# Performance work log

Hardware: AMD Instinct MI355X
Metric: run time of the kernel (lower is better)

Reference implementation:

```python
import jax, jax.numpy as jnp
import numpy as np

B, D_IN, D_OUT, M = 4096, 1024, 1024, 16
GAMMA = 2.0


def setup_inputs() -> dict:
    key = jax.random.key(0)
    ks = jax.random.split(key, 5)
    scale_in = 1.0 / np.sqrt(D_IN)
    return {
        "x": jax.random.normal(ks[0], (B, D_IN), dtype=jnp.float32),
        "W": jax.random.normal(ks[1], (M, D_IN, D_OUT), dtype=jnp.float32) * scale_in,
        "b": jax.random.normal(ks[2], (M, D_OUT), dtype=jnp.float32) * 0.01,
        "Wg": jax.random.normal(ks[3], (D_IN, M), dtype=jnp.float32) * scale_in,
        "bg": jax.random.normal(ks[4], (M,), dtype=jnp.float32) * 0.01,
    }


def reference(x, W, b, Wg, bg):
    # Gate: linear -> pow(gamma) -> normalize by row sum -> relu
    gu = x @ Wg + bg                                   # [B, M]
    gp = jnp.power(gu, GAMMA)                          # gamma = 2.0
    gates = jax.nn.relu(gp / jnp.sum(gp, axis=1, keepdims=True))  # [B, M]
    # M dense expert modules: relu(x @ W_m + b_m), gated and summed (AdditionSublayer)
    h = jax.nn.relu(jnp.einsum("bi,mio->bmo", x, W) + b)          # [B, M, D_OUT]
    return jnp.einsum("bm,bmo->bo", gates, h)                     # [B, D_OUT]
```

## Files before the change

### kernel.cpp

```cpp
#include <hip/hip_runtime.h>

typedef unsigned short u16;
typedef __attribute__((ext_vector_type(4))) float f32x4;
typedef __attribute__((ext_vector_type(8))) short bf16x8;
typedef __attribute__((ext_vector_type(4))) unsigned short u16x4;

#define NT2 256

__device__ __forceinline__ u16 f2bf(float f) {
  union { float f; unsigned u; } v; v.f = f;
  unsigned r = v.u + 0x7FFFu + ((v.u >> 16) & 1u);
  return (u16)(r >> 16);
}

__device__ __forceinline__ f32x4 zero4() {
  f32x4 z; z.x = 0.f; z.y = 0.f; z.z = 0.f; z.w = 0.f; return z;
}

__global__ __launch_bounds__(256) void k_cvt_x(const float* __restrict__ x, u16* __restrict__ xb) {
  int i = blockIdx.x * 256 + threadIdx.x;
  f32x4 v = ((const f32x4*)x)[i];
  u16x4 o;
  o.x = f2bf(v.x); o.y = f2bf(v.y); o.z = f2bf(v.z); o.w = f2bf(v.w);
  ((u16x4*)xb)[i] = o;
}

__global__ __launch_bounds__(256) void k_tw(const float* __restrict__ W, u16* __restrict__ wt) {
  __shared__ float t[64][65];
  int bid = blockIdx.x;
  int e = bid >> 8, rem = bid & 255, kt = rem >> 4, nt = rem & 15;
  int tid = threadIdx.x;
  int lr = tid >> 4, lc4 = (tid & 15) * 4;
  const float* src = W + (size_t)e * 1048576 + (size_t)(kt * 64) * 1024 + nt * 64;
  #pragma unroll
  for (int i = 0; i < 4; ++i) {
    int r = lr + i * 16;
    f32x4 v = *(const f32x4*)(src + (size_t)r * 1024 + lc4);
    t[r][lc4] = v.x; t[r][lc4 + 1] = v.y; t[r][lc4 + 2] = v.z; t[r][lc4 + 3] = v.w;
  }
  __syncthreads();
  int sr = tid >> 3, sc0 = (tid & 7) * 8;
  u16* dst = wt + (size_t)e * 1048576 + (size_t)(nt * 64) * 1024 + kt * 64;
  #pragma unroll
  for (int i = 0; i < 2; ++i) {
    int r2 = sr + i * 32;
    union { u16 u[8]; bf16x8 v; } o;
    #pragma unroll
    for (int j = 0; j < 8; ++j) o.u[j] = f2bf(t[sc0 + j][r2]);
    *(bf16x8*)(dst + (size_t)r2 * 1024 + sc0) = o.v;
  }
}

__global__ __launch_bounds__(256) void k_gates(const float* __restrict__ x, const float* __restrict__ Wg,
                                               const float* __restrict__ bg, float* __restrict__ gates) {
  int wid = threadIdx.x >> 6, lane = threadIdx.x & 63;
  int b = blockIdx.x * 4 + wid;
  const float* xr = x + (size_t)b * 1024;
  float acc[16];
  #pragma unroll
  for (int m = 0; m < 16; ++m) acc[m] = 0.f;
  for (int i0 = lane * 4; i0 < 1024; i0 += 256) {
    f32x4 xv = *(const f32x4*)(xr + i0);
    #pragma unroll
    for (int j = 0; j < 4; ++j) {
      float xs = xv[j];
      const f32x4* wg = (const f32x4*)(Wg + (size_t)(i0 + j) * 16);
      #pragma unroll
      for (int q = 0; q < 4; ++q) {
        f32x4 w = wg[q];
        acc[q*4+0] += xs * w.x; acc[q*4+1] += xs * w.y;
        acc[q*4+2] += xs * w.z; acc[q*4+3] += xs * w.w;
      }
    }
  }
  #pragma unroll
  for (int m = 0; m < 16; ++m) {
    #pragma unroll
    for (int off = 32; off > 0; off >>= 1)
      acc[m] += __shfl_xor(acc[m], off, 64);
  }
  float tot = 0.f, gp[16];
  #pragma unroll
  for (int m = 0; m < 16; ++m) { float gu = acc[m] + bg[m]; gp[m] = gu * gu; tot += gp[m]; }
  float inv = 1.f / tot;
  if (lane == 0) {
    #pragma unroll
    for (int m = 0; m < 16; ++m) gates[(size_t)b * 16 + m] = gp[m] * inv;
  }
}

#define GLL(srcaddr, ldsaddr) \
  __builtin_amdgcn_global_load_lds((const __attribute__((address_space(1))) void*)(srcaddr), \
                                   (__attribute__((address_space(3))) void*)(ldsaddr), 16, 0, 0)

__global__ __launch_bounds__(256, 2)
void k_moe(const u16* __restrict__ xb, const u16* __restrict__ wt,
           const float* __restrict__ gates, const float* __restrict__ bias,
           float* __restrict__ out0, float* __restrict__ p1out) {
  __shared__ __align__(16) u16 sA[3 * 4096];
  __shared__ __align__(16) u16 sB[3 * 4096];
  __shared__ float lgat[1024];
  __shared__ float lbias[1024];

  int tid = threadIdx.x;
  int bid = blockIdx.x;
  int swz = (bid & 7) * 64 + (bid >> 3);
  int btile = swz & 31;
  int pnl = swz >> 5;
  int ntile = pnl & 7;
  int grp = pnl >> 3;
  int brow0 = btile * 128;
  int ncol0 = ntile * 128;
  int mb = grp * 8;

  int wid = tid >> 6, lane = tid & 63;
  int wm = wid >> 1, wn = wid & 1;
  int lrow = lane & 15, lk = lane >> 4;

  const u16* asrc = xb + (size_t)brow0 * 1024;
  const u16* bsrc = wt + (size_t)mb * 1048576 + (size_t)ncol0 * 1024;

  int sg[2], ldd[2];
  #pragma unroll
  for (int it = 0; it < 2; ++it) {
    int idx = it * 256 + tid;
    int r = idx >> 2, s = idx & 3;
    sg[it] = r * 1024 + (s ^ ((r >> 1) & 3)) * 8;
    ldd[it] = (it * 256 + wid * 64) * 8;
  }

  int gsw = lk ^ ((lrow >> 1) & 3);
  int pa = (wm * 64 + lrow) * 32 + gsw * 8;
  int pb = (wn * 64 + lrow) * 32 + gsw * 8;

  f32x4 acc[4][4], oacc[4][4];
  #pragma unroll
  for (int i = 0; i < 4; ++i)
    #pragma unroll
    for (int j = 0; j < 4; ++j) { acc[i][j] = zero4(); oacc[i][j] = zero4(); }

  u16 *a0 = sA, *a1 = sA + 4096, *a2 = sA + 8192;
  u16 *b0 = sB, *b1 = sB + 4096, *b2 = sB + 8192;

  #pragma unroll
  for (int i = 0; i < 4; ++i) {
    int idx = i * 256 + tid;
    lgat[idx] = gates[(size_t)(brow0 + (idx & 127)) * 16 + mb + (idx >> 7)];
    lbias[idx] = bias[(size_t)(mb + (idx >> 7)) * 1024 + ncol0 + (idx & 127)];
  }
  __syncthreads();
  GLL(asrc + sg[0], a0 + ldd[0]); GLL(asrc + sg[1], a0 + ldd[1]);
  GLL(bsrc + sg[0], b0 + ldd[0]); GLL(bsrc + sg[1], b0 + ldd[1]);
  GLL(asrc + 32 + sg[0], a1 + ldd[0]); GLL(asrc + 32 + sg[1], a1 + ldd[1]);
  GLL(bsrc + 32 + sg[0], b1 + ldd[0]); GLL(bsrc + 32 + sg[1], b1 + ldd[1]);
  asm volatile("s_waitcnt vmcnt(4)" ::: "memory");
  __builtin_amdgcn_s_barrier();
  __builtin_amdgcn_sched_barrier(0);

  for (int t = 0; t < NT2; ++t) {
    bf16x8 af0, af1, af2, af3, bf0, bf1, bf2, bf3;
    af0 = *(const bf16x8*)&a0[pa];
    af1 = *(const bf16x8*)&a0[pa + 512];
    af2 = *(const bf16x8*)&a0[pa + 1024];
    af3 = *(const bf16x8*)&a0[pa + 1536];
    bf0 = *(const bf16x8*)&b0[pb];
    bf1 = *(const bf16x8*)&b0[pb + 512];
    bf2 = *(const bf16x8*)&b0[pb + 1024];
    bf3 = *(const bf16x8*)&b0[pb + 1536];

    if (t + 2 < NT2) {
      int t2 = t + 2;
      const u16* sa2 = asrc + (t2 & 31) * 32;
      const u16* sb2 = bsrc + (size_t)(t2 >> 5) * 1048576 + (t2 & 31) * 32;
      GLL(sa2 + sg[0], a2 + ldd[0]); GLL(sa2 + sg[1], a2 + ldd[1]);
      GLL(sb2 + sg[0], b2 + ldd[0]); GLL(sb2 + sg[1], b2 + ldd[1]);
    }

    __builtin_amdgcn_s_setprio(1);
    #pragma unroll
    for (int ni = 0; ni < 4; ++ni) {
      bf16x8 bv = (ni == 0) ? bf0 : (ni == 1) ? bf1 : (ni == 2) ? bf2 : bf3;
      acc[0][ni] = __builtin_amdgcn_mfma_f32_16x16x32_bf16(af0, bv, acc[0][ni], 0, 0, 0);
      acc[1][ni] = __builtin_amdgcn_mfma_f32_16x16x32_bf16(af1, bv, acc[1][ni], 0, 0, 0);
      acc[2][ni] = __builtin_amdgcn_mfma_f32_16x16x32_bf16(af2, bv, acc[2][ni], 0, 0, 0);
      acc[3][ni] = __builtin_amdgcn_mfma_f32_16x16x32_bf16(af3, bv, acc[3][ni], 0, 0, 0);
    }
    __builtin_amdgcn_s_setprio(0);

    if ((t & 31) == 31) {
      int ml = t >> 5;
      float bvv[4];
      #pragma unroll
      for (int ni = 0; ni < 4; ++ni) bvv[ni] = lbias[ml * 128 + wn * 64 + ni * 16 + lrow];
      #pragma unroll
      for (int mi = 0; mi < 4; ++mi) {
        f32x4 gv = *(const f32x4*)&lgat[ml * 128 + wm * 64 + mi * 16 + lk * 4];
        #pragma unroll
        for (int ni = 0; ni < 4; ++ni) {
          #pragma unroll
          for (int j = 0; j < 4; ++j) {
            float h = acc[mi][ni][j] + bvv[ni];
            h = fmaxf(h, 0.f);
            oacc[mi][ni][j] += gv[j] * h;
          }
          acc[mi][ni] = zero4();
        }
      }
    }

    if (t < NT2 - 2)       asm volatile("s_waitcnt vmcnt(4)" ::: "memory");
    else if (t == NT2 - 2) asm volatile("s_waitcnt vmcnt(0)" ::: "memory");
    if (t < NT2 - 1) {
      __builtin_amdgcn_s_barrier();
      __builtin_amdgcn_sched_barrier(0);
      u16* ta = a0; a0 = a1; a1 = a2; a2 = ta;
      u16* tb = b0; b0 = b1; b1 = b2; b2 = tb;
    }
  }

  float* op = grp ? p1out : out0;
  #pragma unroll
  for (int mi = 0; mi < 4; ++mi)
    #pragma unroll
    for (int j = 0; j < 4; ++j) {
      int row = brow0 + wm * 64 + mi * 16 + lk * 4 + j;
      #pragma unroll
      for (int ni = 0; ni < 4; ++ni) {
        int col = ncol0 + wn * 64 + ni * 16 + lrow;
        op[(size_t)row * 1024 + col] = oacc[mi][ni][j];
      }
    }
}

__global__ __launch_bounds__(256) void k_add(float* __restrict__ out, const float* __restrict__ p1) {
  int i = blockIdx.x * 256 + threadIdx.x;
  f32x4 a = ((const f32x4*)out)[i];
  f32x4 b = ((const f32x4*)p1)[i];
  ((f32x4*)out)[i] = a + b;
}

extern "C" void kernel_launch(void* const* d_in, const int* in_sizes, int n_in,
                              void* d_out, int out_size, void* d_ws, size_t ws_size,
                              hipStream_t stream) {
  const float* x  = (const float*)d_in[0];
  const float* W  = (const float*)d_in[1];
  const float* b  = (const float*)d_in[2];
  const float* Wg = (const float*)d_in[3];
  const float* bg = (const float*)d_in[4];
  float* out = (float*)d_out;

  char* ws = (char*)d_ws;
  u16* xb     = (u16*)ws;
  u16* wt     = (u16*)(ws + 8388608);
  float* gts  = (float*)(ws + 41943040);
  float* p1   = (float*)(ws + 42205184);

  k_cvt_x<<<4096, 256, 0, stream>>>(x, xb);
  k_tw<<<4096, 256, 0, stream>>>(W, wt);
  k_gates<<<1024, 256, 0, stream>>>(x, Wg, bg, gts);
  k_moe<<<512, 256, 0, stream>>>(xb, wt, gts, b, out, p1);
  k_add<<<4096, 256, 0, stream>>>(out, p1);
}
```

Baseline: 217.9 us.

## Enlarge MoE GEMM block tile to 256x128 with 8 waves and K=64 stages

The fused expert GEMM now uses 512-thread blocks that each compute a 256-row by 128-column output tile with a 64-wide K step per pipeline stage, instead of 128x128 tiles with K=32. The LDS swizzle moves to 8 chunks per row, and each wave computes a 128x32 sub-tile in two K halves per iteration. The aim is more operand reuse per LDS byte and fewer barriers and iterations. In exchange, LDS use grows to about 156 KB per block, which likely allows only one block per CU despite launch_bounds(512,2). The grid shrinks to 256 blocks, and per-thread register pressure rises from holding eight A fragments.

```diff
diff --git a/kernel.cpp b/kernel.cpp
--- a/kernel.cpp
+++ b/kernel.cpp
@@ -5,7 +5,7 @@
 typedef __attribute__((ext_vector_type(8))) short bf16x8;
 typedef __attribute__((ext_vector_type(4))) unsigned short u16x4;
 
-#define NT2 256
+#define NT 128
 
 __device__ __forceinline__ u16 f2bf(float f) {
   union { float f; unsigned u; } v; v.f = f;
@@ -93,110 +93,135 @@
   __builtin_amdgcn_global_load_lds((const __attribute__((address_space(1))) void*)(srcaddr), \
                                    (__attribute__((address_space(3))) void*)(ldsaddr), 16, 0, 0)
 
-__global__ __launch_bounds__(256, 2)
+__global__ __launch_bounds__(512, 2)
 void k_moe(const u16* __restrict__ xb, const u16* __restrict__ wt,
            const float* __restrict__ gates, const float* __restrict__ bias,
            float* __restrict__ out0, float* __restrict__ p1out) {
-  __shared__ __align__(16) u16 sA[3 * 4096];
-  __shared__ __align__(16) u16 sB[3 * 4096];
-  __shared__ float lgat[1024];
+  __shared__ __align__(16) u16 sA[3 * 16384];
+  __shared__ __align__(16) u16 sB[3 * 8192];
+  __shared__ float lgat[2048];
   __shared__ float lbias[1024];
 
   int tid = threadIdx.x;
   int bid = blockIdx.x;
-  int swz = (bid & 7) * 64 + (bid >> 3);
-  int btile = swz & 31;
-  int pnl = swz >> 5;
+  int swz = (bid & 7) * 32 + (bid >> 3);
+  int btile = swz & 15;
+  int pnl = swz >> 4;
   int ntile = pnl & 7;
   int grp = pnl >> 3;
-  int brow0 = btile * 128;
+  int brow0 = btile * 256;
   int ncol0 = ntile * 128;
   int mb = grp * 8;
 
   int wid = tid >> 6, lane = tid & 63;
-  int wm = wid >> 1, wn = wid & 1;
+  int wm = wid >> 2, wn = wid & 3;
   int lrow = lane & 15, lk = lane >> 4;
+  int sw = lrow & 7;
 
   const u16* asrc = xb + (size_t)brow0 * 1024;
   const u16* bsrc = wt + (size_t)mb * 1048576 + (size_t)ncol0 * 1024;
 
-  int sg[2], ldd[2];
+  int sgA[4], ldA[4], sgB[2], ldB[2];
+  #pragma unroll
+  for (int it = 0; it < 4; ++it) {
+    int idx = it * 512 + tid;
+    int r = idx >> 3, s = idx & 7;
+    sgA[it] = r * 1024 + (s ^ (r & 7)) * 8;
+    ldA[it] = (it * 512 + wid * 64) * 8;
+  }
   #pragma unroll
   for (int it = 0; it < 2; ++it) {
-    int idx = it * 256 + tid;
-    int r = idx >> 2, s = idx & 3;
-    sg[it] = r * 1024 + (s ^ ((r >> 1) & 3)) * 8;
-    ldd[it] = (it * 256 + wid * 64) * 8;
-  }
-
-  int gsw = lk ^ ((lrow >> 1) & 3);
-  int pa = (wm * 64 + lrow) * 32 + gsw * 8;
-  int pb = (wn * 64 + lrow) * 32 + gsw * 8;
-
-  f32x4 acc[4][4], oacc[4][4];
-  #pragma unroll
-  for (int i = 0; i < 4; ++i)
-    #pragma unroll
-    for (int j = 0; j < 4; ++j) { acc[i][j] = zero4(); oacc[i][j] = zero4(); }
-
-  u16 *a0 = sA, *a1 = sA + 4096, *a2 = sA + 8192;
-  u16 *b0 = sB, *b1 = sB + 4096, *b2 = sB + 8192;
+    int idx = it * 512 + tid;
+    int r = idx >> 3, s = idx & 7;
+    sgB[it] = r * 1024 + (s ^ (r & 7)) * 8;
+    ldB[it] = (it * 512 + wid * 64) * 8;
+  }
+
+  int ra[8], rb[2];
+  #pragma unroll
+  for (int mi = 0; mi < 8; ++mi) ra[mi] = (wm * 128 + mi * 16 + lrow) * 64;
+  #pragma unroll
+  for (int ni = 0; ni < 2; ++ni) rb[ni] = (wn * 32 + ni * 16 + lrow) * 64;
+  int pk0 = ((0 + lk) ^ sw) * 8;
+  int pk1 = ((4 + lk) ^ sw) * 8;
+
+  f32x4 acc[8][2], oacc[8][2];
+  #pragma unroll
+  for (int i = 0; i < 8; ++i)
+    #pragma unroll
+    for (int j = 0; j < 2; ++j) { acc[i][j] = zero4(); oacc[i][j] = zero4(); }
+
+  u16 *a0 = sA, *a1 = sA + 16384, *a2 = sA + 32768;
+  u16 *b0 = sB, *b1 = sB + 8192, *b2 = sB + 16384;
 
   #pragma unroll
   for (int i = 0; i < 4; ++i) {
-    int idx = i * 256 + tid;
-    lgat[idx] = gates[(size_t)(brow0 + (idx & 127)) * 16 + mb + (idx >> 7)];
+    int idx = i * 512 + tid;
+    lgat[idx] = gates[(size_t)(brow0 + (idx & 255)) * 16 + mb + (idx >> 8)];
+  }
+  #pragma unroll
+  for (int i = 0; i < 2; ++i) {
+    int idx = i * 512 + tid;
     lbias[idx] = bias[(size_t)(mb + (idx >> 7)) * 1024 + ncol0 + (idx & 127)];
   }
   __syncthreads();
-  GLL(asrc + sg[0], a0 + ldd[0]); GLL(asrc + sg[1], a0 + ldd[1]);
-  GLL(bsrc + sg[0], b0 + ldd[0]); GLL(bsrc + sg[1], b0 + ldd[1]);
-  GLL(asrc + 32 + sg[0], a1 + ldd[0]); GLL(asrc + 32 + sg[1], a1 + ldd[1]);
-  GLL(bsrc + 32 + sg[0], b1 + ldd[0]); GLL(bsrc + 32 + sg[1], b1 + ldd[1]);
-  asm volatile("s_waitcnt vmcnt(4)" ::: "memory");
+  GLL(asrc + sgA[0], a0 + ldA[0]); GLL(asrc + sgA[1], a0 + ldA[1]);
+  GLL(asrc + sgA[2], a0 + ldA[2]); GLL(asrc + sgA[3], a0 + ldA[3]);
+  GLL(bsrc + sgB[0], b0 + ldB[0]); GLL(bsrc + sgB[1], b0 + ldB[1]);
+  GLL(asrc + 64 + sgA[0], a1 + ldA[0]); GLL(asrc + 64 + sgA[1], a1 + ldA[1]);
+  GLL(asrc + 64 + sgA[2], a1 + ldA[2]); GLL(asrc + 64 + sgA[3], a1 + ldA[3]);
+  GLL(bsrc + 64 + sgB[0], b1 + ldB[0]); GLL(bsrc + 64 + sgB[1], b1 + ldB[1]);
+  asm volatile("s_waitcnt vmcnt(6)" ::: "memory");
   __builtin_amdgcn_s_barrier();
   __builtin_amdgcn_sched_barrier(0);
 
-  for (int t = 0; t < NT2; ++t) {
-    bf16x8 af0, af1, af2, af3, bf0, bf1, bf2, bf3;
-    af0 = *(const bf16x8*)&a0[pa];
-    af1 = *(const bf16x8*)&a0[pa + 512];
-    af2 = *(const bf16x8*)&a0[pa + 1024];
-    af3 = *(const bf16x8*)&a0[pa + 1536];
-    bf0 = *(const bf16x8*)&b0[pb];
-    bf1 = *(const bf16x8*)&b0[pb + 512];
-    bf2 = *(const bf16x8*)&b0[pb + 1024];
-    bf3 = *(const bf16x8*)&b0[pb + 1536];
-
-    if (t + 2 < NT2) {
+  for (int t = 0; t < NT; ++t) {
+    bf16x8 af[8], bf0, bf1;
+    #pragma unroll
+    for (int mi = 0; mi < 8; ++mi) af[mi] = *(const bf16x8*)&a0[ra[mi] + pk0];
+    bf0 = *(const bf16x8*)&b0[rb[0] + pk0];
+    bf1 = *(const bf16x8*)&b0[rb[1] + pk0];
+
+    if (t + 2 < NT) {
       int t2 = t + 2;
-      const u16* sa2 = asrc + (t2 & 31) * 32;
-      const u16* sb2 = bsrc + (size_t)(t2 >> 5) * 1048576 + (t2 & 31) * 32;
-      GLL(sa2 + sg[0], a2 + ldd[0]); GLL(sa2 + sg[1], a2 + ldd[1]);
-      GLL(sb2 + sg[0], b2 + ldd[0]); GLL(sb2 + sg[1], b2 + ldd[1]);
+      const u16* sa2 = asrc + (t2 & 15) * 64;
+      const u16* sb2 = bsrc + (size_t)(t2 >> 4) * 1048576 + (t2 & 15) * 64;
+      GLL(sa2 + sgA[0], a2 + ldA[0]); GLL(sa2 + sgA[1], a2 + ldA[1]);
+      GLL(sa2 + sgA[2], a2 + ldA[2]); GLL(sa2 + sgA[3], a2 + ldA[3]);
+      GLL(sb2 + sgB[0], b2 + ldB[0]); GLL(sb2 + sgB[1], b2 + ldB[1]);
     }
 
     __builtin_amdgcn_s_setprio(1);
     #pragma unroll
-    for (int ni = 0; ni < 4; ++ni) {
-      bf16x8 bv = (ni == 0) ? bf0 : (ni == 1) ? bf1 : (ni == 2) ? bf2 : bf3;
-      acc[0][ni] = __builtin_amdgcn_mfma_f32_16x16x32_bf16(af0, bv, acc[0][ni], 0, 0, 0);
-      acc[1][ni] = __builtin_amdgcn_mfma_f32_16x16x32_bf16(af1, bv, acc[1][ni], 0, 0, 0);
-      acc[2][ni] = __builtin_amdgcn_mfma_f32_16x16x32_bf16(af2, bv, acc[2][ni], 0, 0, 0);
-      acc[3][ni] = __builtin_amdgcn_mfma_f32_16x16x32_bf16(af3, bv, acc[3][ni], 0, 0, 0);
+    for (int mi = 0; mi < 8; ++mi) {
+      acc[mi][0] = __builtin_amdgcn_mfma_f32_16x16x32_bf16(af[mi], bf0, acc[mi][0], 0, 0, 0);
+      acc[mi][1] = __builtin_amdgcn_mfma_f32_16x16x32_bf16(af[mi], bf1, acc[mi][1], 0, 0, 0);
     }
     __builtin_amdgcn_s_setprio(0);
 
-    if ((t & 31) == 31) {
-      int ml = t >> 5;
-      float bvv[4];
-      #pragma unroll
-      for (int ni = 0; ni < 4; ++ni) bvv[ni] = lbias[ml * 128 + wn * 64 + ni * 16 + lrow];
-      #pragma unroll
-      for (int mi = 0; mi < 4; ++mi) {
-        f32x4 gv = *(const f32x4*)&lgat[ml * 128 + wm * 64 + mi * 16 + lk * 4];
+    #pragma unroll
+    for (int mi = 0; mi < 8; ++mi) af[mi] = *(const bf16x8*)&a0[ra[mi] + pk1];
+    bf0 = *(const bf16x8*)&b0[rb[0] + pk1];
+    bf1 = *(const bf16x8*)&b0[rb[1] + pk1];
+
+    __builtin_amdgcn_s_setprio(1);
+    #pragma unroll
+    for (int mi = 0; mi < 8; ++mi) {
+      acc[mi][0] = __builtin_amdgcn_mfma_f32_16x16x32_bf16(af[mi], bf0, acc[mi][0], 0, 0, 0);
+      acc[mi][1] = __builtin_amdgcn_mfma_f32_16x16x32_bf16(af[mi], bf1, acc[mi][1], 0, 0, 0);
+    }
+    __builtin_amdgcn_s_setprio(0);
+
+    if ((t & 15) == 15) {
+      int ml = t >> 4;
+      float bvv[2];
+      #pragma unroll
+      for (int ni = 0; ni < 2; ++ni) bvv[ni] = lbias[ml * 128 + wn * 32 + ni * 16 + lrow];
+      #pragma unroll
+      for (int mi = 0; mi < 8; ++mi) {
+        f32x4 gv = *(const f32x4*)&lgat[ml * 256 + wm * 128 + mi * 16 + lk * 4];
         #pragma unroll
-        for (int ni = 0; ni < 4; ++ni) {
+        for (int ni = 0; ni < 2; ++ni) {
           #pragma unroll
           for (int j = 0; j < 4; ++j) {
             float h = acc[mi][ni][j] + bvv[ni];
@@ -208,9 +233,9 @@
       }
     }
 
-    if (t < NT2 - 2)       asm volatile("s_waitcnt vmcnt(4)" ::: "memory");
-    else if (t == NT2 - 2) asm volatile("s_waitcnt vmcnt(0)" ::: "memory");
-    if (t < NT2 - 1) {
+    if (t < NT - 2)       asm volatile("s_waitcnt vmcnt(6)" ::: "memory");
+    else if (t == NT - 2) asm volatile("s_waitcnt vmcnt(0)" ::: "memory");
+    if (t < NT - 1) {
       __builtin_amdgcn_s_barrier();
       __builtin_amdgcn_sched_barrier(0);
       u16* ta = a0; a0 = a1; a1 = a2; a2 = ta;
@@ -220,13 +245,13 @@
 
   float* op = grp ? p1out : out0;
   #pragma unroll
-  for (int mi = 0; mi < 4; ++mi)
+  for (int mi = 0; mi < 8; ++mi)
     #pragma unroll
     for (int j = 0; j < 4; ++j) {
-      int row = brow0 + wm * 64 + mi * 16 + lk * 4 + j;
-      #pragma unroll
-      for (int ni = 0; ni < 4; ++ni) {
-        int col = ncol0 + wn * 64 + ni * 16 + lrow;
+      int row = brow0 + wm * 128 + mi * 16 + lk * 4 + j;
+      #pragma unroll
+      for (int ni = 0; ni < 2; ++ni) {
+        int col = ncol0 + wn * 32 + ni * 16 + lrow;
         op[(size_t)row * 1024 + col] = oacc[mi][ni][j];
       }
     }
@@ -258,6 +283,6 @@
   k_cvt_x<<<4096, 256, 0, stream>>>(x, xb);
   k_tw<<<4096, 256, 0, stream>>>(W, wt);
   k_gates<<<1024, 256, 0, stream>>>(x, Wg, bg, gts);
-  k_moe<<<512, 256, 0, stream>>>(xb, wt, gts, b, out, p1);
+  k_moe<<<256, 512, 0, stream>>>(xb, wt, gts, b, out, p1);
   k_add<<<4096, 256, 0, stream>>>(out, p1);
 }
```

Result: faster. 201.4 us (-7.5%).
